# Performance work log

Hardware: AMD Instinct MI355X
Metric: run time of the kernel (lower is better)

Reference implementation:

```python
import jax, jax.numpy as jnp
import numpy as np
import math

D_MODEL = 2048
H = 16
Q_LORA = 1536
KV_LORA = 512
DN = 128   # qk_nope_head_dim
DR = 64    # qk_rope_head_dim
DV = 128   # v_head_dim
B, S = 2, 2048
EPS = 1e-5


def layernorm(x, g, b):
    mu = jnp.mean(x, axis=-1, keepdims=True)
    var = jnp.mean(jnp.square(x - mu), axis=-1, keepdims=True)
    return (x - mu) * jax.lax.rsqrt(var + EPS) * g + b


def rope_cos_sin(position_ids, dim):
    inv_freq = 1.0 / (10000.0 ** (jnp.arange(0, dim, 2, dtype=jnp.float32) / dim))
    ang = position_ids.astype(jnp.float32)[:, None] * inv_freq[None, :]  # [S, dim/2]
    return jnp.cos(ang), jnp.sin(ang)


def apply_rope(x, cos, sin):
    # x: [..., S, ..., dim]; cos/sin broadcastable [..., S, ..., dim/2]
    x1, x2 = jnp.split(x, 2, axis=-1)
    return jnp.concatenate([x1 * cos - x2 * sin, x1 * sin + x2 * cos], axis=-1)


def setup_inputs() -> dict:
    key = jax.random.key(0)
    ks = jax.random.split(key, 8)
    sc = 0.02
    return {
        "hidden_states": jax.random.normal(ks[0], (B, S, D_MODEL), jnp.float32),
        "w_qa": jax.random.normal(ks[1], (Q_LORA, D_MODEL), jnp.float32) * sc,
        "ln_qa_g": jnp.ones((Q_LORA,), jnp.float32),
        "ln_qa_b": jnp.zeros((Q_LORA,), jnp.float32),
        "w_qb": jax.random.normal(ks[2], (H * DN, Q_LORA), jnp.float32) * sc,
        "w_qrope": jax.random.normal(ks[3], (H * DR, Q_LORA), jnp.float32) * sc,
        "w_kva": jax.random.normal(ks[4], (KV_LORA + DR, D_MODEL), jnp.float32) * sc,
        "ln_kva_g": jnp.ones((KV_LORA,), jnp.float32),
        "ln_kva_b": jnp.zeros((KV_LORA,), jnp.float32),
        "w_kvb": jax.random.normal(ks[5], (H * (DN + DV), KV_LORA), jnp.float32) * sc,
        "w_o": jax.random.normal(ks[6], (D_MODEL, H * DV), jnp.float32) * sc,
        "position_ids": jnp.arange(S, dtype=jnp.int32),
    }


def reference(hidden_states, w_qa, ln_qa_g, ln_qa_b, w_qb, w_qrope,
              w_kva, ln_kva_g, ln_kva_b, w_kvb, w_o, position_ids):
    bsz, seq_len, _ = hidden_states.shape

    # --- Q path (low-rank) ---
    q_latent = layernorm(hidden_states @ w_qa.T, ln_qa_g, ln_qa_b)        # [B,S,Q_LORA]
    q_nope = (q_latent @ w_qb.T).reshape(bsz, seq_len, H, DN)             # [B,S,H,DN]
    q_rope = (q_latent @ w_qrope.T).reshape(bsz, seq_len, H, DR)          # [B,S,H,DR]

    # --- absorb k up-projection into q ---
    k_up = w_kvb[: H * DN].reshape(H, DN, KV_LORA)
    v_up = w_kvb[H * DN:].reshape(H, DV, KV_LORA)
    q_abs = jnp.einsum('bshd,hdr->bshr', q_nope, k_up)                    # [B,S,H,R]

    # --- KV latent path ---
    kv_mixed = hidden_states @ w_kva.T                                    # [B,S,R+DR]
    kv_latent = layernorm(kv_mixed[..., :KV_LORA], ln_kva_g, ln_kva_b)    # [B,S,R]
    k_rope = kv_mixed[..., KV_LORA:]                                      # [B,S,DR]

    # --- RoPE ---
    cos, sin = rope_cos_sin(position_ids, DR)                             # [S,DR/2]
    q_rope = apply_rope(q_rope, cos[None, :, None, :], sin[None, :, None, :])
    k_rope = apply_rope(k_rope, cos[None, :, :], sin[None, :, :])

    # --- attention over latent channel (keys shared across heads) ---
    q_full = jnp.concatenate([q_abs, q_rope], axis=-1)                    # [B,S,H,R+DR]
    k_full = jnp.concatenate([kv_latent, k_rope], axis=-1)                # [B,S,R+DR]
    scale = 1.0 / math.sqrt(DN + DR)
    scores = jnp.einsum('bqhc,bkc->bhqk', q_full, k_full) * scale
    probs = jax.nn.softmax(scores, axis=-1)
    attn = jnp.einsum('bhqk,bkr->bhqr', probs, kv_latent)                 # [B,H,S,R]

    # --- absorbed v up-projection + output ---
    attn_v = jnp.einsum('bhqr,hvr->bqhv', attn, v_up)                     # [B,S,H,DV]
    attn_v = attn_v.reshape(bsz, seq_len, H * DV)
    return attn_v @ w_o.T                                                 # [B,S,D_MODEL]
```

## Files before the change

kernel.cpp:

```cpp
#include <hip/hip_runtime.h>
#include <math.h>

#define D_MODEL 2048
#define NH 16
#define Q_LORA 1536
#define KV_LORA 512
#define DN 128
#define DR 64
#define DV 128
#define BB 2
#define SS 2048
#define NROWS (BB*SS)
#define LN_EPS 1e-5f

typedef __attribute__((ext_vector_type(8))) short short8;
typedef __attribute__((ext_vector_type(4))) float f32x4;

__device__ __forceinline__ ushort f2bf(float f) {
    unsigned int u = __float_as_uint(f);
    u = u + 0x7fffu + ((u >> 16) & 1u);
    return (ushort)(u >> 16);
}

__device__ __forceinline__ void cv4(const float* __restrict__ s,
                                    ushort* __restrict__ d, long i) {
    float4 v = ((const float4*)s)[i];
    ushort4 o;
    o.x = f2bf(v.x); o.y = f2bf(v.y); o.z = f2bf(v.z); o.w = f2bf(v.w);
    ((ushort4*)d)[i] = o;
}

__global__ __launch_bounds__(256)
void cvt_all(const float* __restrict__ hs,     const float* __restrict__ w_qa,
             const float* __restrict__ w_qb,   const float* __restrict__ w_qrope,
             const float* __restrict__ w_kvb,  const float* __restrict__ w_kva,
             ushort* __restrict__ hs_bf,       ushort* __restrict__ w_qa_bf,
             ushort* __restrict__ w_qb_bf,     ushort* __restrict__ w_qrope_bf,
             ushort* __restrict__ w_kvb_bf,    ushort* __restrict__ w_kva_bf)
{
    long i = (long)blockIdx.x * 256 + threadIdx.x;
    if (i < 2097152) { cv4(hs, hs_bf, i); return; }
    i -= 2097152;
    if (i < 786432) { cv4(w_qa, w_qa_bf, i); return; }
    i -= 786432;
    if (i < 786432) { cv4(w_qb, w_qb_bf, i); return; }
    i -= 786432;
    if (i < 393216) { cv4(w_qrope, w_qrope_bf, i); return; }
    i -= 393216;
    if (i < 524288) { cv4(w_kvb, w_kvb_bf, i); return; }
    i -= 524288;
    if (i >= 327680) return;
    long e = i * 4;
    int row = (int)(e >> 11), col = (int)(e & 2047);
    ushort4 o;
    if (row < 576) {
        float4 v = *(const float4*)(w_kva + (long)row * 2048 + col);
        o.x = f2bf(v.x); o.y = f2bf(v.y); o.z = f2bf(v.z); o.w = f2bf(v.w);
    } else { o.x = 0; o.y = 0; o.z = 0; o.w = 0; }
    *(ushort4*)(w_kva_bf + (long)row * 2048 + col) = o;
}

__global__ __launch_bounds__(256)
void cvt_bf16(const float* __restrict__ in, ushort* __restrict__ out, long n4)
{
    long i = (long)blockIdx.x * 256 + threadIdx.x;
    if (i >= n4) return;
    cv4(in, out, i);
}

#define GLL16(g, l) \
    __builtin_amdgcn_global_load_lds((const __attribute__((address_space(1))) void*)(g), \
                                     (__attribute__((address_space(3))) void*)(l), 16, 0, 0)

__device__ __forceinline__ void gemm_core(const ushort* __restrict__ A,
    const ushort* __restrict__ Bp, ushort* As, ushort* Bs,
    int K, int lda, int ldb, int m0, int n0, int tid, f32x4 acc[4][4])
{
    int l = tid & 63, w = tid >> 6;
    int l15 = l & 15, quad = l >> 4;
    int wm = (w >> 1) * 64, wn = (w & 1) * 64;
    int ob = tid * 16;
    int row = ob >> 6, colb = ob & 63;
    const char* ga0 = (const char*)(A  + (long)(m0 + row) * lda)      + colb;
    const char* ga1 = (const char*)(A  + (long)(m0 + row + 64) * lda) + colb;
    const char* gb0 = (const char*)(Bp + (long)(n0 + row) * ldb)      + colb;
    const char* gb1 = (const char*)(Bp + (long)(n0 + row + 64) * ldb) + colb;
    ushort* la0 = As + tid * 8;
    ushort* la1 = As + 2048 + tid * 8;
    ushort* lb0 = Bs + tid * 8;
    ushort* lb1 = Bs + 2048 + tid * 8;

    for (int k0 = 0; k0 < K; k0 += 32) {
        GLL16(ga0, la0); GLL16(ga1, la1);
        GLL16(gb0, lb0); GLL16(gb1, lb1);
        ga0 += 64; ga1 += 64; gb0 += 64; gb1 += 64;
        __syncthreads();
        short8 af[4], bf[4];
        #pragma unroll
        for (int i = 0; i < 4; ++i)
            af[i] = *(const short8*)(As + (wm + i * 16 + l15) * 32 + quad * 8);
        #pragma unroll
        for (int j = 0; j < 4; ++j)
            bf[j] = *(const short8*)(Bs + (wn + j * 16 + l15) * 32 + quad * 8);
        #pragma unroll
        for (int i = 0; i < 4; ++i)
            #pragma unroll
            for (int j = 0; j < 4; ++j)
                acc[i][j] = __builtin_amdgcn_mfma_f32_16x16x32_bf16(
                    af[i], bf[j], acc[i][j], 0, 0, 0);
        __syncthreads();
    }
}

__global__ __launch_bounds__(256)
void gemm_f32out(const ushort* __restrict__ A, const ushort* __restrict__ B,
                 float* __restrict__ C, int K, int lda, int ldb, int ldc)
{
    __shared__ __align__(16) ushort As[128 * 32];
    __shared__ __align__(16) ushort Bs[128 * 32];
    int tid = threadIdx.x;
    int m0 = blockIdx.y * 128, n0 = blockIdx.x * 128;
    f32x4 acc[4][4] = {};
    gemm_core(A, B, As, Bs, K, lda, ldb, m0, n0, tid, acc);
    int l = tid & 63, w = tid >> 6;
    int l15 = l & 15, quad = l >> 4;
    int wm = (w >> 1) * 64, wn = (w & 1) * 64;
    #pragma unroll
    for (int i = 0; i < 4; ++i)
        #pragma unroll
        for (int j = 0; j < 4; ++j)
            #pragma unroll
            for (int r = 0; r < 4; ++r) {
                long gm = m0 + wm + i * 16 + quad * 4 + r;
                long gn = n0 + wn + j * 16 + l15;
                C[gm * ldc + gn] = acc[i][j][r];
            }
}

__global__ __launch_bounds__(256)
void gemm_dual(const ushort* __restrict__ A, const ushort* __restrict__ Bqa,
               const ushort* __restrict__ Bkva, float* __restrict__ Cq,
               float* __restrict__ Ckv)
{
    __shared__ __align__(16) ushort As[128 * 32];
    __shared__ __align__(16) ushort Bs[128 * 32];
    int tid = threadIdx.x;
    int bx = blockIdx.x;
    int m0 = blockIdx.y * 128;
    const ushort* Bp; float* C; int ldc, n0;
    if (bx < 12) { n0 = bx * 128;        Bp = Bqa  + (long)n0 * 2048; C = Cq;  ldc = 1536; }
    else         { n0 = (bx - 12) * 128; Bp = Bkva + (long)n0 * 2048; C = Ckv; ldc = 640; }
    f32x4 acc[4][4] = {};
    gemm_core(A, Bp, As, Bs, D_MODEL, D_MODEL, D_MODEL, m0, 0, tid, acc);
    int l = tid & 63, w = tid >> 6;
    int l15 = l & 15, quad = l >> 4;
    int wm = (w >> 1) * 64, wn = (w & 1) * 64;
    #pragma unroll
    for (int i = 0; i < 4; ++i)
        #pragma unroll
        for (int j = 0; j < 4; ++j)
            #pragma unroll
            for (int r = 0; r < 4; ++r) {
                long gm = m0 + wm + i * 16 + quad * 4 + r;
                long gn = n0 + wn + j * 16 + l15;
                C[gm * ldc + gn] = acc[i][j][r];
            }
}

__global__ __launch_bounds__(256)
void gemm_q23(const ushort* __restrict__ A, const ushort* __restrict__ Bqb,
              const ushort* __restrict__ Bqr, ushort* __restrict__ qfull,
              const float2* __restrict__ tab)
{
    __shared__ __align__(16) ushort As[128 * 32];
    __shared__ __align__(16) ushort Bs[128 * 32];
    int tid = threadIdx.x;
    int m0 = blockIdx.y * 128, n0 = blockIdx.x * 128;
    const ushort* Bp = (n0 < 2048) ? Bqb + (long)n0 * Q_LORA
                                   : Bqr + (long)(n0 - 2048) * Q_LORA;
    f32x4 acc[4][4] = {};
    gemm_core(A, Bp, As, Bs, Q_LORA, Q_LORA, Q_LORA, m0, 0, tid, acc);
    int l = tid & 63, w = tid >> 6;
    int l15 = l & 15, quad = l >> 4;
    int wm = (w >> 1) * 64, wn = (w & 1) * 64;
    if (n0 < 2048) {
        int head = n0 >> 7;
        #pragma unroll
        for (int i = 0; i < 4; ++i)
            #pragma unroll
            for (int j = 0; j < 4; ++j)
                #pragma unroll
                for (int r = 0; r < 4; ++r) {
                    long gm = m0 + wm + i * 16 + quad * 4 + r;
                    int c = wn + j * 16 + l15;
                    qfull[(gm * NH + head) * 192 + c] = f2bf(acc[i][j][r]);
                }
    } else {
        int nb = n0 - 2048;
        int head = (nb + wn) >> 6;
        #pragma unroll
        for (int i = 0; i < 4; ++i)
            #pragma unroll
            for (int j = 0; j < 2; ++j)
                #pragma unroll
                for (int r = 0; r < 4; ++r) {
                    long gm = m0 + wm + i * 16 + quad * 4 + r;
                    int ir = j * 16 + l15;
                    int s = (int)(gm & (SS - 1));
                    float2 cs = tab[s * 32 + ir];
                    float x1 = acc[i][j][r], x2 = acc[i][j + 2][r];
                    ushort* op = qfull + (gm * NH + head) * 192 + 128;
                    op[ir]      = f2bf(x1 * cs.x - x2 * cs.y);
                    op[ir + 32] = f2bf(x1 * cs.y + x2 * cs.x);
                }
    }
}

__global__ __launch_bounds__(256)
void gemm_kv56(const ushort* __restrict__ A, const ushort* __restrict__ B,
               ushort* __restrict__ kfull, ushort* __restrict__ vt)
{
    __shared__ __align__(16) ushort As[128 * 32];
    __shared__ __align__(16) ushort Bs[128 * 32];
    int tid = threadIdx.x;
    int m0 = blockIdx.y * 128, n0 = blockIdx.x * 128;
    const ushort* Bp = B + (long)n0 * KV_LORA;
    f32x4 acc[4][4] = {};
    gemm_core(A, Bp, As, Bs, KV_LORA, KV_LORA, KV_LORA, m0, 0, tid, acc);
    int l = tid & 63, w = tid >> 6;
    int l15 = l & 15, quad = l >> 4;
    int wm = (w >> 1) * 64, wn = (w & 1) * 64;
    if (n0 < 2048) {
        int head = n0 >> 7;
        #pragma unroll
        for (int i = 0; i < 4; ++i)
            #pragma unroll
            for (int j = 0; j < 4; ++j)
                #pragma unroll
                for (int r = 0; r < 4; ++r) {
                    long gm = m0 + wm + i * 16 + quad * 4 + r;
                    int c = wn + j * 16 + l15;
                    kfull[(gm * NH + head) * 192 + c] = f2bf(acc[i][j][r]);
                }
    } else {
        int head = (n0 >> 7) - 16;
        #pragma unroll
        for (int i = 0; i < 4; ++i)
            #pragma unroll
            for (int j = 0; j < 4; ++j) {
                long gm0 = m0 + wm + i * 16 + quad * 4;
                int c = wn + j * 16 + l15;
                ushort4 p;
                p.x = f2bf(acc[i][j][0]); p.y = f2bf(acc[i][j][1]);
                p.z = f2bf(acc[i][j][2]); p.w = f2bf(acc[i][j][3]);
                *(ushort4*)(vt + (long)head * 128 * 4096 + (long)c * 4096 + gm0) = p;
            }
    }
}

__global__ __launch_bounds__(256)
void ln_rows_bf(const float* __restrict__ in, ushort* __restrict__ out,
                const float* __restrict__ g, const float* __restrict__ b,
                int n, int ld_in, int ld_out)
{
    long rowi = blockIdx.x;
    const float* x = in + rowi * ld_in;
    ushort* y = out + rowi * ld_out;
    int tid = threadIdx.x;
    float s = 0.f, ss = 0.f;
    for (int i = tid; i < n; i += 256) { float v = x[i]; s += v; ss += v * v; }
    #pragma unroll
    for (int off = 32; off > 0; off >>= 1) {
        s  += __shfl_xor(s, off);
        ss += __shfl_xor(ss, off);
    }
    __shared__ float sred[4], ssred[4];
    int wid = tid >> 6, lane = tid & 63;
    if (lane == 0) { sred[wid] = s; ssred[wid] = ss; }
    __syncthreads();
    s  = sred[0] + sred[1] + sred[2] + sred[3];
    ss = ssred[0] + ssred[1] + ssred[2] + ssred[3];
    float mu  = s / n;
    float var = ss / n - mu * mu;
    float r = 1.0f / sqrtf(var + LN_EPS);
    for (int i = tid; i < n; i += 256)
        y[i] = f2bf((x[i] - mu) * r * g[i] + b[i]);
}

__global__ __launch_bounds__(256)
void rope_tab_k(const int* __restrict__ pos, float2* __restrict__ tab)
{
    int idx = blockIdx.x * 256 + threadIdx.x;
    if (idx >= SS * 32) return;
    int i = idx & 31;
    int s = idx >> 5;
    double ang = (double)pos[s] * exp(-(double)i * 0.28782313662425572);
    float2 cs;
    cs.x = (float)cos(ang);
    cs.y = (float)sin(ang);
    tab[idx] = cs;
}

__global__ __launch_bounds__(256)
void rope_k(const float* __restrict__ kvm, ushort* __restrict__ kfull,
            const float2* __restrict__ tab)
{
    long idx = (long)blockIdx.x * 256 + threadIdx.x;
    if (idx >= (long)NROWS * 32) return;
    int i = (int)(idx & 31);
    long rowi = idx >> 5;
    int s = (int)(rowi & (SS - 1));
    float2 cs = tab[s * 32 + i];
    float c = cs.x, sn = cs.y;
    const float* p = kvm + rowi * 640 + 512;
    float x1 = p[i], x2 = p[i + 32];
    ushort v1 = f2bf(x1 * c - x2 * sn);
    ushort v2 = f2bf(x1 * sn + x2 * c);
    ushort* o = kfull + rowi * NH * 192 + 128;
    #pragma unroll
    for (int h = 0; h < NH; ++h) {
        o[h * 192 + i]      = v1;
        o[h * 192 + i + 32] = v2;
    }
}

#define FSCALE 0.07216878364870322f

__global__ __launch_bounds__(512, 4)
void flash_mfma(const ushort* __restrict__ qf, const ushort* __restrict__ kf,
                const ushort* __restrict__ vt, ushort* __restrict__ attnv)
{
    __shared__ __align__(16) ushort Ks[64 * 192];
    __shared__ __align__(16) ushort Vs[144 * 64];
    __shared__ __align__(16) ushort Ps[128 * 72];
    int tid = threadIdx.x;
    int w = tid >> 6, l = tid & 63, l15 = l & 15, quad = l >> 4;
    int bh = blockIdx.x;
    int b = bh >> 4, h = bh & 15;
    int q0 = blockIdx.y * 128;

    {
        int e = 8192 + tid * 2;
        ushort2 iv;
        iv.x = (e     < 8256) ? (ushort)0x3F80 : (ushort)0;
        iv.y = (e + 1 < 8256) ? (ushort)0x3F80 : (ushort)0;
        *(ushort2*)&Vs[e] = iv;
    }

    const ushort* qp = qf + ((long)(b * SS + q0 + 16 * w + l15) * NH + h) * 192 + quad * 8;
    short8 aq[6];
    #pragma unroll
    for (int kk = 0; kk < 6; ++kk) aq[kk] = *(const short8*)(qp + kk * 32);

    f32x4 o[8] = {};
    f32x4 osum = {};
    float mrow = -INFINITY;

    const ushort* kbase = kf + ((long)(b * SS) * NH + h) * 192;
    const ushort* vbase = vt + (long)h * 128 * 4096 + (long)b * SS;

    int r0k = tid >> 3, subk = tid & 7;
    int v0  = tid >> 2, subv = tid & 3;
    const ushort* kgp = kbase + (long)r0k * (NH * 192);
    const ushort* vgp = vbase + (long)v0 * 4096;

    short8 pk[3], pv[2];
    #pragma unroll
    for (int it = 0; it < 3; ++it)
        pk[it] = *(const short8*)(kgp + (subk + 8 * it) * 8);
    #pragma unroll
    for (int it = 0; it < 2; ++it)
        pv[it] = *(const short8*)(vgp + (subv + 4 * it) * 8);

    int ksw = r0k & 7, vsw = v0 & 7;

    for (int k0 = 0; k0 < SS; k0 += 64) {
        __syncthreads();
        #pragma unroll
        for (int it = 0; it < 3; ++it)
            *(short8*)&Ks[r0k * 192 + ((subk + 8 * it) ^ ksw) * 8] = pk[it];
        #pragma unroll
        for (int it = 0; it < 2; ++it)
            *(short8*)&Vs[v0 * 64 + ((subv + 4 * it) ^ vsw) * 8] = pv[it];
        __syncthreads();
        if (k0 + 64 < SS) {
            const ushort* kg = kgp + (long)(k0 + 64) * (NH * 192);
            const ushort* vg = vgp + (k0 + 64);
            #pragma unroll
            for (int it = 0; it < 3; ++it)
                pk[it] = *(const short8*)(kg + (subk + 8 * it) * 8);
            #pragma unroll
            for (int it = 0; it < 2; ++it)
                pv[it] = *(const short8*)(vg + (subv + 4 * it) * 8);
        }

        f32x4 sc[4] = {};
        __builtin_amdgcn_s_setprio(1);
        #pragma unroll
        for (int kk = 0; kk < 6; ++kk) {
            #pragma unroll
            for (int j = 0; j < 4; ++j) {
                int krow = j * 16 + l15;
                short8 kfr = *(const short8*)&Ks[krow * 192 + (((kk * 4 + quad) ^ (krow & 7))) * 8];
                sc[j] = __builtin_amdgcn_mfma_f32_16x16x32_bf16(kfr, aq[kk], sc[j], 0, 0, 0);
            }
        }
        __builtin_amdgcn_s_setprio(0);

        float rmax = fmaxf(
            fmaxf(fmaxf(fmaxf(sc[0][0], sc[0][1]), fmaxf(sc[0][2], sc[0][3])),
                  fmaxf(fmaxf(sc[1][0], sc[1][1]), fmaxf(sc[1][2], sc[1][3]))),
            fmaxf(fmaxf(fmaxf(sc[2][0], sc[2][1]), fmaxf(sc[2][2], sc[2][3])),
                  fmaxf(fmaxf(sc[3][0], sc[3][1]), fmaxf(sc[3][2], sc[3][3]))));
        rmax = fmaxf(rmax, __shfl_xor(rmax, 16));
        rmax = fmaxf(rmax, __shfl_xor(rmax, 32));
        float pmax = rmax * FSCALE;

        if (__any(pmax > mrow + 8.0f)) {
            float mnew = fmaxf(mrow, pmax);
            float alpha = __expf(mrow - mnew);
            mrow = mnew;
            float a0 = __shfl(alpha, quad * 4 + 0);
            float a1 = __shfl(alpha, quad * 4 + 1);
            float a2 = __shfl(alpha, quad * 4 + 2);
            float a3 = __shfl(alpha, quad * 4 + 3);
            #pragma unroll
            for (int v8 = 0; v8 < 8; ++v8) {
                o[v8][0] *= a0; o[v8][1] *= a1;
                o[v8][2] *= a2; o[v8][3] *= a3;
            }
            osum[0] *= a0; osum[1] *= a1; osum[2] *= a2; osum[3] *= a3;
        }

        int prow = (16 * w + l15) * 72 + quad * 4;
        #pragma unroll
        for (int j = 0; j < 4; ++j) {
            float p0 = __expf(fmaf(sc[j][0], FSCALE, -mrow));
            float p1 = __expf(fmaf(sc[j][1], FSCALE, -mrow));
            float p2 = __expf(fmaf(sc[j][2], FSCALE, -mrow));
            float p3 = __expf(fmaf(sc[j][3], FSCALE, -mrow));
            uint2 pu;
            pu.x = (uint)f2bf(p0) | ((uint)f2bf(p1) << 16);
            pu.y = (uint)f2bf(p2) | ((uint)f2bf(p3) << 16);
            *(uint2*)&Ps[prow + j * 16] = pu;
        }

        __builtin_amdgcn_s_setprio(1);
        #pragma unroll
        for (int ks = 0; ks < 2; ++ks) {
            short8 pa = *(const short8*)&Ps[(16 * w + l15) * 72 + ks * 32 + quad * 8];
            #pragma unroll
            for (int v8 = 0; v8 < 8; ++v8) {
                int vrow = v8 * 16 + l15;
                short8 bv = *(const short8*)&Vs[vrow * 64 + (((ks * 4 + quad) ^ (vrow & 7))) * 8];
                o[v8] = __builtin_amdgcn_mfma_f32_16x16x32_bf16(pa, bv, o[v8], 0, 0, 0);
            }
            {
                int vrow = 128 + l15;
                short8 bv = *(const short8*)&Vs[vrow * 64 + (((ks * 4 + quad) ^ (vrow & 7))) * 8];
                osum = __builtin_amdgcn_mfma_f32_16x16x32_bf16(pa, bv, osum, 0, 0, 0);
            }
        }
        __builtin_amdgcn_s_setprio(0);
    }

    #pragma unroll
    for (int r = 0; r < 4; ++r) {
        float lsum = __shfl(osum[r], l & 48);
        float inv = 1.0f / lsum;
        long rowi = (long)(b * SS) + q0 + 16 * w + quad * 4 + r;
        ushort* op = attnv + (rowi * NH + h) * 128;
        #pragma unroll
        for (int v8 = 0; v8 < 8; ++v8)
            op[v8 * 16 + l15] = f2bf(o[v8][r] * inv);
    }
}


extern "C" void kernel_launch(void* const* d_in, const int* in_sizes, int n_in,
                              void* d_out, int out_size, void* d_ws, size_t ws_size,
                              hipStream_t stream) {
    const float* hs       = (const float*)d_in[0];
    const float* w_qa     = (const float*)d_in[1];
    const float* ln_qa_g  = (const float*)d_in[2];
    const float* ln_qa_b  = (const float*)d_in[3];
    const float* w_qb     = (const float*)d_in[4];
    const float* w_qrope  = (const float*)d_in[5];
    const float* w_kva    = (const float*)d_in[6];
    const float* ln_kva_g = (const float*)d_in[7];
    const float* ln_kva_b = (const float*)d_in[8];
    const float* w_kvb    = (const float*)d_in[9];
    const float* w_o      = (const float*)d_in[10];
    const int*   pos      = (const int*)d_in[11];
    float* out = (float*)d_out;

    char* W = (char*)d_ws;
    ushort* hs_bf     = (ushort*)(W + 0);
    ushort* w_o_bf    = (ushort*)(W + 0);
    ushort* w_qa_bf   = (ushort*)(W + 16777216);
    ushort* w_qb_bf   = (ushort*)(W + 23068672);
    ushort* w_qrope_bf= (ushort*)(W + 29360128);
    ushort* w_kva_bf  = (ushort*)(W + 32505856);
    ushort* w_kvb_bf  = (ushort*)(W + 35127296);
    float*  q_lat_f   = (float*)(W + 39321600);
    ushort* q_lat_bf  = (ushort*)(W + 64487424);
    float*  kv_mix    = (float*)(W + 77070336);
    ushort* kv_lat_bf = (ushort*)(W + 87556096);
    ushort* q_full    = (ushort*)(W + 91750400);
    ushort* k_full    = (ushort*)(W + 116916224);
    ushort* v_exp_t   = (ushort*)(W + 142082048);
    ushort* attnv_bf  = (ushort*)(W + 158859264);
    float2* rope_tab  = (float2*)(W + 158859264);

    dim3 blk(256);

    rope_tab_k<<<dim3(256), blk, 0, stream>>>(pos, rope_tab);
    cvt_all<<<dim3(19200), blk, 0, stream>>>(
        hs, w_qa, w_qb, w_qrope, w_kvb, w_kva,
        hs_bf, w_qa_bf, w_qb_bf, w_qrope_bf, w_kvb_bf, w_kva_bf);
    gemm_dual<<<dim3(17, 32), blk, 0, stream>>>(
        hs_bf, w_qa_bf, w_kva_bf, q_lat_f, kv_mix);
    cvt_bf16<<<dim3(4096), blk, 0, stream>>>(w_o, w_o_bf, 1048576);
    ln_rows_bf<<<dim3(NROWS), blk, 0, stream>>>(
        q_lat_f, q_lat_bf, ln_qa_g, ln_qa_b, Q_LORA, Q_LORA, Q_LORA);
    ln_rows_bf<<<dim3(NROWS), blk, 0, stream>>>(
        kv_mix, kv_lat_bf, ln_kva_g, ln_kva_b, KV_LORA, 640, KV_LORA);
    rope_k<<<dim3(512), blk, 0, stream>>>(kv_mix, k_full, rope_tab);
    gemm_q23<<<dim3(24, 32), blk, 0, stream>>>(
        q_lat_bf, w_qb_bf, w_qrope_bf, q_full, rope_tab);
    gemm_kv56<<<dim3(32, 32), blk, 0, stream>>>(
        kv_lat_bf, w_kvb_bf, k_full, v_exp_t);
    flash_mfma<<<dim3(BB * NH, SS / 128), dim3(512), 0, stream>>>(
        q_full, k_full, v_exp_t, attnv_bf);
    gemm_f32out<<<dim3(16, 32), blk, 0, stream>>>(
        attnv_bf, w_o_bf, out, NH * DV, NH * DV, NH * DV, D_MODEL);
}
```

Measured before the change: 519.3 us.

## Merge small kernels into fewer launches and use exp2 in flash softmax

Folds the rope-table build into the conversion kernel, merges both layernorms, the k-rope and the w_o conversion into one launch, and merges the Q and KV up-projection GEMMs into a single grid. In the flash kernel, the scale is folded into a log2 factor so the softmax uses a native exp2 instead of __expf, with the rescale threshold converted to match. This cuts launch overhead and gaps between dependent kernels and lets the two GEMMs share the GPU, at the cost of branchy heterogeneous blocks.

```diff
diff --git a/kernel.cpp b/kernel.cpp
--- a/kernel.cpp
+++ b/kernel.cpp
@@ -22,6 +22,14 @@
     return (ushort)(u >> 16);
 }
 
+__device__ __forceinline__ float fexp2(float x) {
+#if __has_builtin(__builtin_amdgcn_exp2f)
+    return __builtin_amdgcn_exp2f(x);
+#else
+    return exp2f(x);
+#endif
+}
+
 __device__ __forceinline__ void cv4(const float* __restrict__ s,
                                     ushort* __restrict__ d, long i) {
     float4 v = ((const float4*)s)[i];
@@ -36,7 +44,8 @@
              const float* __restrict__ w_kvb,  const float* __restrict__ w_kva,
              ushort* __restrict__ hs_bf,       ushort* __restrict__ w_qa_bf,
              ushort* __restrict__ w_qb_bf,     ushort* __restrict__ w_qrope_bf,
-             ushort* __restrict__ w_kvb_bf,    ushort* __restrict__ w_kva_bf)
+             ushort* __restrict__ w_kvb_bf,    ushort* __restrict__ w_kva_bf,
+             const int* __restrict__ pos,      float2* __restrict__ tab)
 {
     long i = (long)blockIdx.x * 256 + threadIdx.x;
     if (i < 2097152) { cv4(hs, hs_bf, i); return; }
@@ -49,23 +58,27 @@
     i -= 393216;
     if (i < 524288) { cv4(w_kvb, w_kvb_bf, i); return; }
     i -= 524288;
-    if (i >= 327680) return;
-    long e = i * 4;
-    int row = (int)(e >> 11), col = (int)(e & 2047);
-    ushort4 o;
-    if (row < 576) {
-        float4 v = *(const float4*)(w_kva + (long)row * 2048 + col);
-        o.x = f2bf(v.x); o.y = f2bf(v.y); o.z = f2bf(v.z); o.w = f2bf(v.w);
-    } else { o.x = 0; o.y = 0; o.z = 0; o.w = 0; }
-    *(ushort4*)(w_kva_bf + (long)row * 2048 + col) = o;
-}
-
-__global__ __launch_bounds__(256)
-void cvt_bf16(const float* __restrict__ in, ushort* __restrict__ out, long n4)
-{
-    long i = (long)blockIdx.x * 256 + threadIdx.x;
-    if (i >= n4) return;
-    cv4(in, out, i);
+    if (i < 327680) {
+        long e = i * 4;
+        int row = (int)(e >> 11), col = (int)(e & 2047);
+        ushort4 o;
+        if (row < 576) {
+            float4 v = *(const float4*)(w_kva + (long)row * 2048 + col);
+            o.x = f2bf(v.x); o.y = f2bf(v.y); o.z = f2bf(v.z); o.w = f2bf(v.w);
+        } else { o.x = 0; o.y = 0; o.z = 0; o.w = 0; }
+        *(ushort4*)(w_kva_bf + (long)row * 2048 + col) = o;
+        return;
+    }
+    i -= 327680;
+    if (i >= 65536) return;
+    int idx = (int)i;
+    int fi = idx & 31;
+    int s = idx >> 5;
+    double ang = (double)pos[s] * exp(-(double)fi * 0.28782313662425572);
+    float2 cs;
+    cs.x = (float)cos(ang);
+    cs.y = (float)sin(ang);
+    tab[idx] = cs;
 }
 
 #define GLL16(g, l) \
@@ -168,163 +181,156 @@
 }
 
 __global__ __launch_bounds__(256)
-void gemm_q23(const ushort* __restrict__ A, const ushort* __restrict__ Bqb,
+void gemm_qkv(const ushort* __restrict__ Aq, const ushort* __restrict__ Bqb,
               const ushort* __restrict__ Bqr, ushort* __restrict__ qfull,
-              const float2* __restrict__ tab)
+              const float2* __restrict__ tab,
+              const ushort* __restrict__ Akv, const ushort* __restrict__ Bkvb,
+              ushort* __restrict__ kfull, ushort* __restrict__ vt)
 {
     __shared__ __align__(16) ushort As[128 * 32];
     __shared__ __align__(16) ushort Bs[128 * 32];
     int tid = threadIdx.x;
-    int m0 = blockIdx.y * 128, n0 = blockIdx.x * 128;
-    const ushort* Bp = (n0 < 2048) ? Bqb + (long)n0 * Q_LORA
-                                   : Bqr + (long)(n0 - 2048) * Q_LORA;
-    f32x4 acc[4][4] = {};
-    gemm_core(A, Bp, As, Bs, Q_LORA, Q_LORA, Q_LORA, m0, 0, tid, acc);
+    int bx = blockIdx.x;
+    int m0 = blockIdx.y * 128;
     int l = tid & 63, w = tid >> 6;
     int l15 = l & 15, quad = l >> 4;
     int wm = (w >> 1) * 64, wn = (w & 1) * 64;
-    if (n0 < 2048) {
-        int head = n0 >> 7;
-        #pragma unroll
-        for (int i = 0; i < 4; ++i)
-            #pragma unroll
-            for (int j = 0; j < 4; ++j)
+    f32x4 acc[4][4] = {};
+
+    if (bx < 24) {
+        int n0 = bx * 128;
+        const ushort* Bp = (n0 < 2048) ? Bqb + (long)n0 * Q_LORA
+                                       : Bqr + (long)(n0 - 2048) * Q_LORA;
+        gemm_core(Aq, Bp, As, Bs, Q_LORA, Q_LORA, Q_LORA, m0, 0, tid, acc);
+        if (n0 < 2048) {
+            int head = n0 >> 7;
+            #pragma unroll
+            for (int i = 0; i < 4; ++i)
                 #pragma unroll
-                for (int r = 0; r < 4; ++r) {
-                    long gm = m0 + wm + i * 16 + quad * 4 + r;
+                for (int j = 0; j < 4; ++j)
+                    #pragma unroll
+                    for (int r = 0; r < 4; ++r) {
+                        long gm = m0 + wm + i * 16 + quad * 4 + r;
+                        int c = wn + j * 16 + l15;
+                        qfull[(gm * NH + head) * 192 + c] = f2bf(acc[i][j][r]);
+                    }
+        } else {
+            int nb = n0 - 2048;
+            int head = (nb + wn) >> 6;
+            #pragma unroll
+            for (int i = 0; i < 4; ++i)
+                #pragma unroll
+                for (int j = 0; j < 2; ++j)
+                    #pragma unroll
+                    for (int r = 0; r < 4; ++r) {
+                        long gm = m0 + wm + i * 16 + quad * 4 + r;
+                        int ir = j * 16 + l15;
+                        int s = (int)(gm & (SS - 1));
+                        float2 cs = tab[s * 32 + ir];
+                        float x1 = acc[i][j][r], x2 = acc[i][j + 2][r];
+                        ushort* op = qfull + (gm * NH + head) * 192 + 128;
+                        op[ir]      = f2bf(x1 * cs.x - x2 * cs.y);
+                        op[ir + 32] = f2bf(x1 * cs.y + x2 * cs.x);
+                    }
+        }
+    } else {
+        int n0 = (bx - 24) * 128;
+        const ushort* Bp = Bkvb + (long)n0 * KV_LORA;
+        gemm_core(Akv, Bp, As, Bs, KV_LORA, KV_LORA, KV_LORA, m0, 0, tid, acc);
+        if (n0 < 2048) {
+            int head = n0 >> 7;
+            #pragma unroll
+            for (int i = 0; i < 4; ++i)
+                #pragma unroll
+                for (int j = 0; j < 4; ++j)
+                    #pragma unroll
+                    for (int r = 0; r < 4; ++r) {
+                        long gm = m0 + wm + i * 16 + quad * 4 + r;
+                        int c = wn + j * 16 + l15;
+                        kfull[(gm * NH + head) * 192 + c] = f2bf(acc[i][j][r]);
+                    }
+        } else {
+            int head = (n0 >> 7) - 16;
+            #pragma unroll
+            for (int i = 0; i < 4; ++i)
+                #pragma unroll
+                for (int j = 0; j < 4; ++j) {
+                    long gm0 = m0 + wm + i * 16 + quad * 4;
                     int c = wn + j * 16 + l15;
-                    qfull[(gm * NH + head) * 192 + c] = f2bf(acc[i][j][r]);
+                    ushort4 p;
+                    p.x = f2bf(acc[i][j][0]); p.y = f2bf(acc[i][j][1]);
+                    p.z = f2bf(acc[i][j][2]); p.w = f2bf(acc[i][j][3]);
+                    *(ushort4*)(vt + (long)head * 128 * 4096 + (long)c * 4096 + gm0) = p;
                 }
-    } else {
-        int nb = n0 - 2048;
-        int head = (nb + wn) >> 6;
-        #pragma unroll
-        for (int i = 0; i < 4; ++i)
-            #pragma unroll
-            for (int j = 0; j < 2; ++j)
-                #pragma unroll
-                for (int r = 0; r < 4; ++r) {
-                    long gm = m0 + wm + i * 16 + quad * 4 + r;
-                    int ir = j * 16 + l15;
-                    int s = (int)(gm & (SS - 1));
-                    float2 cs = tab[s * 32 + ir];
-                    float x1 = acc[i][j][r], x2 = acc[i][j + 2][r];
-                    ushort* op = qfull + (gm * NH + head) * 192 + 128;
-                    op[ir]      = f2bf(x1 * cs.x - x2 * cs.y);
-                    op[ir + 32] = f2bf(x1 * cs.y + x2 * cs.x);
-                }
+        }
     }
 }
 
 __global__ __launch_bounds__(256)
-void gemm_kv56(const ushort* __restrict__ A, const ushort* __restrict__ B,
-               ushort* __restrict__ kfull, ushort* __restrict__ vt)
-{
-    __shared__ __align__(16) ushort As[128 * 32];
-    __shared__ __align__(16) ushort Bs[128 * 32];
-    int tid = threadIdx.x;
-    int m0 = blockIdx.y * 128, n0 = blockIdx.x * 128;
-    const ushort* Bp = B + (long)n0 * KV_LORA;
-    f32x4 acc[4][4] = {};
-    gemm_core(A, Bp, As, Bs, KV_LORA, KV_LORA, KV_LORA, m0, 0, tid, acc);
-    int l = tid & 63, w = tid >> 6;
-    int l15 = l & 15, quad = l >> 4;
-    int wm = (w >> 1) * 64, wn = (w & 1) * 64;
-    if (n0 < 2048) {
-        int head = n0 >> 7;
-        #pragma unroll
-        for (int i = 0; i < 4; ++i)
-            #pragma unroll
-            for (int j = 0; j < 4; ++j)
-                #pragma unroll
-                for (int r = 0; r < 4; ++r) {
-                    long gm = m0 + wm + i * 16 + quad * 4 + r;
-                    int c = wn + j * 16 + l15;
-                    kfull[(gm * NH + head) * 192 + c] = f2bf(acc[i][j][r]);
-                }
-    } else {
-        int head = (n0 >> 7) - 16;
-        #pragma unroll
-        for (int i = 0; i < 4; ++i)
-            #pragma unroll
-            for (int j = 0; j < 4; ++j) {
-                long gm0 = m0 + wm + i * 16 + quad * 4;
-                int c = wn + j * 16 + l15;
-                ushort4 p;
-                p.x = f2bf(acc[i][j][0]); p.y = f2bf(acc[i][j][1]);
-                p.z = f2bf(acc[i][j][2]); p.w = f2bf(acc[i][j][3]);
-                *(ushort4*)(vt + (long)head * 128 * 4096 + (long)c * 4096 + gm0) = p;
-            }
-    }
-}
-
-__global__ __launch_bounds__(256)
-void ln_rows_bf(const float* __restrict__ in, ushort* __restrict__ out,
-                const float* __restrict__ g, const float* __restrict__ b,
-                int n, int ld_in, int ld_out)
-{
-    long rowi = blockIdx.x;
-    const float* x = in + rowi * ld_in;
-    ushort* y = out + rowi * ld_out;
-    int tid = threadIdx.x;
-    float s = 0.f, ss = 0.f;
-    for (int i = tid; i < n; i += 256) { float v = x[i]; s += v; ss += v * v; }
-    #pragma unroll
-    for (int off = 32; off > 0; off >>= 1) {
-        s  += __shfl_xor(s, off);
-        ss += __shfl_xor(ss, off);
-    }
+void ln_rope(const float* __restrict__ qlf, ushort* __restrict__ qlbf,
+             const float* __restrict__ gqa, const float* __restrict__ bqa,
+             const float* __restrict__ kvm, ushort* __restrict__ kvbf,
+             const float* __restrict__ gkv, const float* __restrict__ bkv,
+             ushort* __restrict__ kfull, const float2* __restrict__ tab,
+             const float* __restrict__ w_o, ushort* __restrict__ w_o_bf)
+{
     __shared__ float sred[4], ssred[4];
-    int wid = tid >> 6, lane = tid & 63;
-    if (lane == 0) { sred[wid] = s; ssred[wid] = ss; }
-    __syncthreads();
-    s  = sred[0] + sred[1] + sred[2] + sred[3];
-    ss = ssred[0] + ssred[1] + ssred[2] + ssred[3];
-    float mu  = s / n;
-    float var = ss / n - mu * mu;
-    float r = 1.0f / sqrtf(var + LN_EPS);
-    for (int i = tid; i < n; i += 256)
-        y[i] = f2bf((x[i] - mu) * r * g[i] + b[i]);
-}
-
-__global__ __launch_bounds__(256)
-void rope_tab_k(const int* __restrict__ pos, float2* __restrict__ tab)
-{
-    int idx = blockIdx.x * 256 + threadIdx.x;
-    if (idx >= SS * 32) return;
-    int i = idx & 31;
-    int s = idx >> 5;
-    double ang = (double)pos[s] * exp(-(double)i * 0.28782313662425572);
-    float2 cs;
-    cs.x = (float)cos(ang);
-    cs.y = (float)sin(ang);
-    tab[idx] = cs;
-}
-
-__global__ __launch_bounds__(256)
-void rope_k(const float* __restrict__ kvm, ushort* __restrict__ kfull,
-            const float2* __restrict__ tab)
-{
-    long idx = (long)blockIdx.x * 256 + threadIdx.x;
-    if (idx >= (long)NROWS * 32) return;
-    int i = (int)(idx & 31);
-    long rowi = idx >> 5;
-    int s = (int)(rowi & (SS - 1));
-    float2 cs = tab[s * 32 + i];
-    float c = cs.x, sn = cs.y;
-    const float* p = kvm + rowi * 640 + 512;
-    float x1 = p[i], x2 = p[i + 32];
-    ushort v1 = f2bf(x1 * c - x2 * sn);
-    ushort v2 = f2bf(x1 * sn + x2 * c);
-    ushort* o = kfull + rowi * NH * 192 + 128;
-    #pragma unroll
-    for (int h = 0; h < NH; ++h) {
-        o[h * 192 + i]      = v1;
-        o[h * 192 + i + 32] = v2;
-    }
-}
-
-#define FSCALE 0.07216878364870322f
+    int bid = blockIdx.x, tid = threadIdx.x;
+    if (bid < 2 * NROWS) {
+        const float* x; ushort* y; const float* g; const float* b; int n;
+        if (bid < NROWS) {
+            x = qlf + (long)bid * Q_LORA; y = qlbf + (long)bid * Q_LORA;
+            g = gqa; b = bqa; n = Q_LORA;
+        } else {
+            int r = bid - NROWS;
+            x = kvm + (long)r * 640; y = kvbf + (long)r * KV_LORA;
+            g = gkv; b = bkv; n = KV_LORA;
+        }
+        float s = 0.f, ss = 0.f;
+        for (int i = tid; i < n; i += 256) { float v = x[i]; s += v; ss += v * v; }
+        #pragma unroll
+        for (int off = 32; off > 0; off >>= 1) {
+            s  += __shfl_xor(s, off);
+            ss += __shfl_xor(ss, off);
+        }
+        int wid = tid >> 6, lane = tid & 63;
+        if (lane == 0) { sred[wid] = s; ssred[wid] = ss; }
+        __syncthreads();
+        s  = sred[0] + sred[1] + sred[2] + sred[3];
+        ss = ssred[0] + ssred[1] + ssred[2] + ssred[3];
+        float mu  = s / n;
+        float var = ss / n - mu * mu;
+        float r = 1.0f / sqrtf(var + LN_EPS);
+        for (int i = tid; i < n; i += 256)
+            y[i] = f2bf((x[i] - mu) * r * g[i] + b[i]);
+        return;
+    }
+    if (bid < 2 * NROWS + 512) {
+        long idx = (long)(bid - 2 * NROWS) * 256 + tid;
+        if (idx >= (long)NROWS * 32) return;
+        int i = (int)(idx & 31);
+        long rowi = idx >> 5;
+        int s = (int)(rowi & (SS - 1));
+        float2 cs = tab[s * 32 + i];
+        float c = cs.x, sn = cs.y;
+        const float* p = kvm + rowi * 640 + 512;
+        float x1 = p[i], x2 = p[i + 32];
+        ushort v1 = f2bf(x1 * c - x2 * sn);
+        ushort v2 = f2bf(x1 * sn + x2 * c);
+        ushort* o = kfull + rowi * NH * 192 + 128;
+        #pragma unroll
+        for (int h = 0; h < NH; ++h) {
+            o[h * 192 + i]      = v1;
+            o[h * 192 + i + 32] = v2;
+        }
+        return;
+    }
+    long i = (long)(bid - (2 * NROWS + 512)) * 256 + tid;
+    if (i < 1048576) cv4(w_o, w_o_bf, i);
+}
+
+#define C2LOG 0.10412700456539414f
+#define THR2  11.541560327111707f
 
 __global__ __launch_bounds__(512, 4)
 void flash_mfma(const ushort* __restrict__ qf, const ushort* __restrict__ kf,
@@ -414,11 +420,11 @@
                   fmaxf(fmaxf(sc[3][0], sc[3][1]), fmaxf(sc[3][2], sc[3][3]))));
         rmax = fmaxf(rmax, __shfl_xor(rmax, 16));
         rmax = fmaxf(rmax, __shfl_xor(rmax, 32));
-        float pmax = rmax * FSCALE;
-
-        if (__any(pmax > mrow + 8.0f)) {
+        float pmax = rmax * C2LOG;
+
+        if (__any(pmax > mrow + THR2)) {
             float mnew = fmaxf(mrow, pmax);
-            float alpha = __expf(mrow - mnew);
+            float alpha = fexp2(mrow - mnew);
             mrow = mnew;
             float a0 = __shfl(alpha, quad * 4 + 0);
             float a1 = __shfl(alpha, quad * 4 + 1);
@@ -435,10 +441,10 @@
         int prow = (16 * w + l15) * 72 + quad * 4;
         #pragma unroll
         for (int j = 0; j < 4; ++j) {
-            float p0 = __expf(fmaf(sc[j][0], FSCALE, -mrow));
-            float p1 = __expf(fmaf(sc[j][1], FSCALE, -mrow));
-            float p2 = __expf(fmaf(sc[j][2], FSCALE, -mrow));
-            float p3 = __expf(fmaf(sc[j][3], FSCALE, -mrow));
+            float p0 = fexp2(fmaf(sc[j][0], C2LOG, -mrow));
+            float p1 = fexp2(fmaf(sc[j][1], C2LOG, -mrow));
+            float p2 = fexp2(fmaf(sc[j][2], C2LOG, -mrow));
+            float p3 = fexp2(fmaf(sc[j][3], C2LOG, -mrow));
             uint2 pu;
             pu.x = (uint)f2bf(p0) | ((uint)f2bf(p1) << 16);
             pu.y = (uint)f2bf(p2) | ((uint)f2bf(p3) << 16);
@@ -514,21 +520,18 @@
 
     dim3 blk(256);
 
-    rope_tab_k<<<dim3(256), blk, 0, stream>>>(pos, rope_tab);
-    cvt_all<<<dim3(19200), blk, 0, stream>>>(
+    cvt_all<<<dim3(19456), blk, 0, stream>>>(
         hs, w_qa, w_qb, w_qrope, w_kvb, w_kva,
-        hs_bf, w_qa_bf, w_qb_bf, w_qrope_bf, w_kvb_bf, w_kva_bf);
+        hs_bf, w_qa_bf, w_qb_bf, w_qrope_bf, w_kvb_bf, w_kva_bf,
+        pos, rope_tab);
     gemm_dual<<<dim3(17, 32), blk, 0, stream>>>(
         hs_bf, w_qa_bf, w_kva_bf, q_lat_f, kv_mix);
-    cvt_bf16<<<dim3(4096), blk, 0, stream>>>(w_o, w_o_bf, 1048576);
-    ln_rows_bf<<<dim3(NROWS), blk, 0, stream>>>(
-        q_lat_f, q_lat_bf, ln_qa_g, ln_qa_b, Q_LORA, Q_LORA, Q_LORA);
-    ln_rows_bf<<<dim3(NROWS), blk, 0, stream>>>(
-        kv_mix, kv_lat_bf, ln_kva_g, ln_kva_b, KV_LORA, 640, KV_LORA);
-    rope_k<<<dim3(512), blk, 0, stream>>>(kv_mix, k_full, rope_tab);
-    gemm_q23<<<dim3(24, 32), blk, 0, stream>>>(
-        q_lat_bf, w_qb_bf, w_qrope_bf, q_full, rope_tab);
-    gemm_kv56<<<dim3(32, 32), blk, 0, stream>>>(
+    ln_rope<<<dim3(12800), blk, 0, stream>>>(
+        q_lat_f, q_lat_bf, ln_qa_g, ln_qa_b,
+        kv_mix, kv_lat_bf, ln_kva_g, ln_kva_b,
+        k_full, rope_tab, w_o, w_o_bf);
+    gemm_qkv<<<dim3(56, 32), blk, 0, stream>>>(
+        q_lat_bf, w_qb_bf, w_qrope_bf, q_full, rope_tab,
         kv_lat_bf, w_kvb_bf, k_full, v_exp_t);
     flash_mfma<<<dim3(BB * NH, SS / 128), dim3(512), 0, stream>>>(
         q_full, k_full, v_exp_t, attnv_bf);
```

After: 503.7 us. 1.03x faster.
